# Kernel optimization log

Hardware: AMD Instinct MI355X
Metric: run time of the kernel (lower is better)

Reference implementation:

```python
import jax, jax.numpy as jnp
import numpy as np

MIN_CLUSTERS = 3.0
MAX_CLUSTERS = 50.0


def setup_inputs() -> dict:
    key = jax.random.key(0)
    ks = jax.random.split(key, 12)
    B, N, D = 16, 8192, 256
    E_half = B * N * 16  # avg degree ~32 after symmetrization
    x = jax.random.normal(ks[0], (B, N, D), dtype=jnp.float32)
    mask = jnp.zeros((B, 1, N), dtype=jnp.float32)  # all nodes valid (> -1e8)
    # within-graph random edges, duplicated in both directions (undirected convention)
    g = jax.random.randint(ks[1], (E_half,), 0, B)
    u = jax.random.randint(ks[2], (E_half,), 0, N)
    v = jax.random.randint(ks[3], (E_half,), 0, N)
    src = (g * N + u).astype(jnp.int32)
    dst = (g * N + v).astype(jnp.int32)
    edge_index = jnp.stack([jnp.concatenate([src, dst]), jnp.concatenate([dst, src])])
    batch_vec = jnp.repeat(jnp.arange(B, dtype=jnp.int32), N)
    x_graph = jax.random.normal(ks[4], (B * N, 64), dtype=jnp.float32)
    in_dim = 3 * D + 5  # 773
    W1 = jax.random.normal(ks[5], (in_dim, 64), dtype=jnp.float32) * 0.02
    b1 = jnp.zeros((64,), dtype=jnp.float32)
    W2 = jax.random.normal(ks[6], (64, 32), dtype=jnp.float32) * 0.02
    b2 = jnp.zeros((32,), dtype=jnp.float32)
    W3 = jax.random.normal(ks[7], (32, 1), dtype=jnp.float32) * 0.02
    b3 = jnp.zeros((1,), dtype=jnp.float32)
    return {"x": x, "mask": mask, "x_graph": x_graph, "edge_index": edge_index,
            "batch_vec": batch_vec, "W1": W1, "b1": b1, "W2": W2, "b2": b2,
            "W3": W3, "b3": b3}


def reference(x, mask, x_graph, edge_index, batch_vec, W1, b1, W2, b2, W3, b3):
    B, N, D = x.shape
    valid = mask[:, 0, :] > -1e8  # [B, N] bool
    vf = valid.astype(x.dtype)
    node_counts = vf.sum(axis=1)               # [B]
    safe_nc = jnp.maximum(node_counts, 1.0)
    max_allowed = jnp.minimum(safe_nc, MAX_CLUSTERS)
    min_allowed = jnp.minimum(max_allowed, MIN_CLUSTERS)

    # masked pooled node-feature stats (mean / max / unbiased std)
    cnt = node_counts[:, None]                  # [B,1]
    x_mean = (x * vf[:, :, None]).sum(axis=1) / jnp.maximum(cnt, 1.0)
    x_max = jnp.where(valid[:, :, None], x, -jnp.inf).max(axis=1)
    x_max = jnp.where(cnt > 0, x_max, 0.0)
    diff = (x - x_mean[:, None, :]) * vf[:, :, None]
    var = (diff * diff).sum(axis=1) / jnp.maximum(cnt - 1.0, 1.0)
    x_std = jnp.where(cnt > 1, jnp.sqrt(var), 0.0)

    # structural features: degree histogram via one segment_sum over edge endpoints
    src, dst = edge_index[0], edge_index[1]
    total_nodes = batch_vec.shape[0]
    same = (batch_vec[src] == batch_vec[dst]).astype(x.dtype)
    deg = jax.ops.segment_sum(same, src, num_segments=total_nodes)  # per-node degree
    nodes_per_graph = jax.ops.segment_sum(jnp.ones((total_nodes,), x.dtype), batch_vec, num_segments=B)
    E_b = jax.ops.segment_sum(same, batch_vec[src], num_segments=B)
    num_edges = jnp.floor(E_b / 2.0)  # edge_index duplicated both directions -> E//2
    deg_sum = jax.ops.segment_sum(deg, batch_vec, num_segments=B)
    deg_sq = jax.ops.segment_sum(deg * deg, batch_vec, num_segments=B)
    deg_max = jax.ops.segment_max(deg, batch_vec, num_segments=B)
    npg = jnp.maximum(nodes_per_graph, 1.0)
    deg_mean = deg_sum / npg
    deg_var = (deg_sq - nodes_per_graph * deg_mean * deg_mean) / jnp.maximum(nodes_per_graph - 1.0, 1.0)
    deg_std = jnp.sqrt(jnp.maximum(deg_var, 0.0))

    nc = node_counts
    max_edges = nc * (nc - 1.0) / 2.0
    has = (E_b > 0) & (nc > 1)
    density = jnp.where(has, num_edges / jnp.maximum(max_edges, 1.0), 0.0)
    avg_degree = jnp.where(has, deg_mean / 10.0, 0.0)
    max_degree = jnp.where(has, deg_max / jnp.maximum(nc, 1.0), 0.0)
    degree_std = jnp.where(has & (nodes_per_graph > 1), deg_std / 10.0, 0.0)
    log_size = jnp.log(nc + 1.0) / 5.0
    structural = jnp.stack([log_size, density, avg_degree, max_degree, degree_std], axis=1)

    gf = jnp.concatenate([x_mean, x_max, x_std, structural], axis=1)  # [B, 3D+5]
    h = jax.nn.relu(gf @ W1 + b1)          # dropout is identity at inference
    h = jax.nn.relu(h @ W2 + b2)
    score = jax.nn.sigmoid(h @ W3 + b3)[:, 0]

    ncc = MIN_CLUSTERS + score * (MAX_CLUSTERS - MIN_CLUSTERS)
    ncc = jnp.maximum(jnp.minimum(ncc, max_allowed), min_allowed)
    rounded = jnp.round(ncc)
    max_batch_clusters = max_allowed.min().astype(jnp.int32)
    num_clusters_final = jnp.clip(rounded.mean().astype(jnp.int32), 1, max_batch_clusters)
    cluster_ratio = (ncc / safe_nc).mean()
    return num_clusters_final, cluster_ratio
```

## Files before the change

kernel.cpp:

```cpp
#include <hip/hip_runtime.h>
#include <math.h>

#define BATCH  16
#define NDIM   8192
#define NSHIFT 13
#define DDIM   256
#define NS2    64
#define TCNT   81


__global__ void __launch_bounds__(512) k_edge(
        const int* __restrict__ e0, const int* __restrict__ e1,
        const int* __restrict__ bv, int* __restrict__ gacc,
        unsigned char* __restrict__ hist, int E, int ce, int NH, int total_nodes) {
    __shared__ unsigned hloc[16384];
    __shared__ int sflag;
    int tid = threadIdx.x, bid = blockIdx.x;
    if (bid == 0 && tid < 128) gacc[tid] = 0;
    if (tid == 0) sflag = 0;
    #pragma unroll
    for (int i = 0; i < 32; ++i) hloc[tid + 512 * i] = 0u;
    {
        const int4* bv4 = (const int4*)bv;
        int n4 = total_nodes >> 2;
        int bad = 0;
        for (int i = tid; i < n4; i += 512) {
            int4 v = bv4[i];
            int g = (i * 4) >> NSHIFT;
            bad |= (v.x ^ g) | (v.y ^ g) | (v.z ^ g) | (v.w ^ g);
        }
        if (bad) atomicOr(&sflag, 1);
    }
    __syncthreads();
    bool fp = (sflag == 0);
    int h = bid % NH, c = bid / NH;
    int start = c * ce;
    int end = start + ce; if (end > E) end = E;
    if (fp) {
        for (int e = start + tid * 4; e + 3 < end; e += 512 * 4) {
            int4 s4 = *(const int4*)(e0 + e);
            int4 d4 = *(const int4*)(e1 + e);
            if ((s4.x >> NSHIFT) == (d4.x >> NSHIFT) && (s4.x >> 16) == h)
                atomicAdd(&hloc[(s4.x & 65535) >> 2], 1u << ((s4.x & 3) * 8));
            if ((s4.y >> NSHIFT) == (d4.y >> NSHIFT) && (s4.y >> 16) == h)
                atomicAdd(&hloc[(s4.y & 65535) >> 2], 1u << ((s4.y & 3) * 8));
            if ((s4.z >> NSHIFT) == (d4.z >> NSHIFT) && (s4.z >> 16) == h)
                atomicAdd(&hloc[(s4.z & 65535) >> 2], 1u << ((s4.z & 3) * 8));
            if ((s4.w >> NSHIFT) == (d4.w >> NSHIFT) && (s4.w >> 16) == h)
                atomicAdd(&hloc[(s4.w & 65535) >> 2], 1u << ((s4.w & 3) * 8));
        }
    } else {
        for (int e = start + tid * 4; e + 3 < end; e += 512 * 4) {
            int4 s4 = *(const int4*)(e0 + e);
            int4 d4 = *(const int4*)(e1 + e);
            if (bv[s4.x] == bv[d4.x] && (s4.x >> 16) == h)
                atomicAdd(&hloc[(s4.x & 65535) >> 2], 1u << ((s4.x & 3) * 8));
            if (bv[s4.y] == bv[d4.y] && (s4.y >> 16) == h)
                atomicAdd(&hloc[(s4.y & 65535) >> 2], 1u << ((s4.y & 3) * 8));
            if (bv[s4.z] == bv[d4.z] && (s4.z >> 16) == h)
                atomicAdd(&hloc[(s4.z & 65535) >> 2], 1u << ((s4.z & 3) * 8));
            if (bv[s4.w] == bv[d4.w] && (s4.w >> 16) == h)
                atomicAdd(&hloc[(s4.w & 65535) >> 2], 1u << ((s4.w & 3) * 8));
        }
    }
    __syncthreads();
    uint4* dst = (uint4*)(hist + (size_t)c * ((size_t)NH * 65536) + (size_t)h * 65536);
    const uint4* src = (const uint4*)hloc;
    #pragma unroll
    for (int i = 0; i < 8; ++i) dst[tid + 512 * i] = src[tid + 512 * i];
}

__global__ void __launch_bounds__(256) k_work(
        const unsigned char* __restrict__ hist, const int* __restrict__ bv,
        const float* __restrict__ x, const float* __restrict__ mask,
        float* __restrict__ part, int* __restrict__ vcarr, int* __restrict__ gacc,
        int total_nodes, int NCHUNK, int NH, int MRGB) {
    __shared__ float4 Ls[256], Lq[256], Lm[256];
    __shared__ unsigned pk[4][64][8];
    __shared__ int ls[BATCH], lq[BATCH], lm[BATCH], lc[BATCH], lvc;
    int t = threadIdx.x;
    if ((int)blockIdx.x < MRGB) {
        if (t < BATCH) { ls[t] = 0; lq[t] = 0; lm[t] = 0; lc[t] = 0; }
        int cg = t >> 6, col = t & 63;
        int gcol = blockIdx.x * 64 + col;
        int nCol = total_nodes >> 4;
        unsigned a0=0,a1=0,a2=0,a3=0,b0=0,b1=0,b2=0,b3=0;
        if (gcol < nCol) {
            const uint4* H4 = (const uint4*)hist;
            size_t SB4 = ((size_t)NH * 65536) >> 4;
            #pragma unroll 2
            for (int c = cg; c < NCHUNK; c += 4) {
                uint4 v = H4[(size_t)c * SB4 + gcol];
                a0 += v.x & 0x00FF00FFu; b0 += (v.x >> 8) & 0x00FF00FFu;
                a1 += v.y & 0x00FF00FFu; b1 += (v.y >> 8) & 0x00FF00FFu;
                a2 += v.z & 0x00FF00FFu; b2 += (v.z >> 8) & 0x00FF00FFu;
                a3 += v.w & 0x00FF00FFu; b3 += (v.w >> 8) & 0x00FF00FFu;
            }
        }
        pk[cg][col][0] = a0; pk[cg][col][1] = a1; pk[cg][col][2] = a2; pk[cg][col][3] = a3;
        pk[cg][col][4] = b0; pk[cg][col][5] = b1; pk[cg][col][6] = b2; pk[cg][col][7] = b3;
        __syncthreads();
        int col2 = t >> 2, w = t & 3;
        int node0 = blockIdx.x * 1024 + col2 * 16 + w * 4;
        if (node0 + 3 < total_nodes) {
            unsigned A = pk[0][col2][w]     + pk[1][col2][w]     + pk[2][col2][w]     + pk[3][col2][w];
            unsigned B = pk[0][col2][4 + w] + pk[1][col2][4 + w] + pk[2][col2][4 + w] + pk[3][col2][4 + w];
            int c0 = (int)(A & 0xFFFFu), c2 = (int)(A >> 16);
            int c1 = (int)(B & 0xFFFFu), c3 = (int)(B >> 16);
            int4 bq = ((const int4*)bv)[node0 >> 2];
            if (bq.x == bq.y && bq.x == bq.z && bq.x == bq.w) {
                int b = bq.x;
                int mx = max(max(c0, c1), max(c2, c3));
                atomicAdd(&ls[b], c0 + c1 + c2 + c3);
                atomicAdd(&lq[b], c0 * c0 + c1 * c1 + c2 * c2 + c3 * c3);
                atomicMax(&lm[b], mx);
                atomicAdd(&lc[b], 4);
            } else {
                int cc[4] = { c0, c1, c2, c3 };
                int bb[4] = { bq.x, bq.y, bq.z, bq.w };
                for (int k = 0; k < 4; ++k) {
                    atomicAdd(&ls[bb[k]], cc[k]);
                    atomicAdd(&lq[bb[k]], cc[k] * cc[k]);
                    atomicMax(&lm[bb[k]], cc[k]);
                    atomicAdd(&lc[bb[k]], 1);
                }
            }
        }
        __syncthreads();
        if (t < BATCH) {
            if (ls[t]) atomicAdd(&gacc[t], ls[t]);
            if (lq[t]) atomicAdd(&gacc[BATCH + t], lq[t]);
            if (lm[t]) atomicMax(&gacc[2 * BATCH + t], lm[t]);
            if (lc[t]) atomicAdd(&gacc[3 * BATCH + t], lc[t]);
        }
    } else {
        int idx = blockIdx.x - MRGB;
        int ns = idx & (NS2 - 1), b = idx / NS2;
        int dbase = (t & 63) * 4, rg = t >> 6;
        int n0 = ns * (NDIM / NS2);
        const float* prow = x + (size_t)b * NDIM * DDIM + (size_t)(n0 + rg) * DDIM + dbase;
        const float* pm   = mask + (size_t)b * NDIM + n0 + rg;
        float s0=0.f,s1=0.f,s2=0.f,s3=0.f;
        float q0=0.f,q1=0.f,q2=0.f,q3=0.f;
        float m0=-INFINITY,m1=-INFINITY,m2=-INFINITY,m3=-INFINITY;
        int vcnt = 0;
        #pragma unroll 2
        for (int k = 0; k < 8; ++k) {
            float4 v0 = *(const float4*)(prow);
            float4 v1 = *(const float4*)(prow + 4 * DDIM);
            float4 v2 = *(const float4*)(prow + 8 * DDIM);
            float4 v3 = *(const float4*)(prow + 12 * DDIM);
            float f0 = (pm[0]  > -1.0e8f) ? 1.f : 0.f;
            float f1 = (pm[4]  > -1.0e8f) ? 1.f : 0.f;
            float f2 = (pm[8]  > -1.0e8f) ? 1.f : 0.f;
            float f3 = (pm[12] > -1.0e8f) ? 1.f : 0.f;
            s0 += v0.x*f0 + v1.x*f1 + v2.x*f2 + v3.x*f3;
            s1 += v0.y*f0 + v1.y*f1 + v2.y*f2 + v3.y*f3;
            s2 += v0.z*f0 + v1.z*f1 + v2.z*f2 + v3.z*f3;
            s3 += v0.w*f0 + v1.w*f1 + v2.w*f2 + v3.w*f3;
            q0 += v0.x*v0.x*f0 + v1.x*v1.x*f1 + v2.x*v2.x*f2 + v3.x*v3.x*f3;
            q1 += v0.y*v0.y*f0 + v1.y*v1.y*f1 + v2.y*v2.y*f2 + v3.y*v3.y*f3;
            q2 += v0.z*v0.z*f0 + v1.z*v1.z*f1 + v2.z*v2.z*f2 + v3.z*v3.z*f3;
            q3 += v0.w*v0.w*f0 + v1.w*v1.w*f1 + v2.w*v2.w*f2 + v3.w*v3.w*f3;
            if (f0 > 0.f) { m0=fmaxf(m0,v0.x); m1=fmaxf(m1,v0.y); m2=fmaxf(m2,v0.z); m3=fmaxf(m3,v0.w); }
            if (f1 > 0.f) { m0=fmaxf(m0,v1.x); m1=fmaxf(m1,v1.y); m2=fmaxf(m2,v1.z); m3=fmaxf(m3,v1.w); }
            if (f2 > 0.f) { m0=fmaxf(m0,v2.x); m1=fmaxf(m1,v2.y); m2=fmaxf(m2,v2.z); m3=fmaxf(m3,v2.w); }
            if (f3 > 0.f) { m0=fmaxf(m0,v3.x); m1=fmaxf(m1,v3.y); m2=fmaxf(m2,v3.z); m3=fmaxf(m3,v3.w); }
            vcnt += (int)f0 + (int)f1 + (int)f2 + (int)f3;
            prow += 16 * DDIM;
            pm   += 16;
        }
        if (t == 0) lvc = 0;
        Ls[t] = make_float4(s0, s1, s2, s3);
        Lq[t] = make_float4(q0, q1, q2, q3);
        Lm[t] = make_float4(m0, m1, m2, m3);
        __syncthreads();
        if ((t & 63) == 0 && vcnt) atomicAdd(&lvc, vcnt);
        if (t < 64) {
            float4 S = Ls[t], Q = Lq[t], M = Lm[t];
            #pragma unroll
            for (int r = 1; r < 4; ++r) {
                float4 a = Ls[t + 64 * r];
                S.x += a.x; S.y += a.y; S.z += a.z; S.w += a.w;
                a = Lq[t + 64 * r];
                Q.x += a.x; Q.y += a.y; Q.z += a.z; Q.w += a.w;
                a = Lm[t + 64 * r];
                M.x = fmaxf(M.x, a.x); M.y = fmaxf(M.y, a.y);
                M.z = fmaxf(M.z, a.z); M.w = fmaxf(M.w, a.w);
            }
            size_t base = ((size_t)(b * NS2 + ns) * 3) * DDIM;
            *(float4*)(part + base + 0 * DDIM + 4 * t) = S;
            *(float4*)(part + base + 1 * DDIM + 4 * t) = Q;
            *(float4*)(part + base + 2 * DDIM + 4 * t) = M;
        }
        __syncthreads();
        if (t == 0) vcarr[idx] = lvc;
    }
}

__global__ void __launch_bounds__(256) k_tail(
        const float* __restrict__ part, const int* __restrict__ vcarr,
        int* __restrict__ gacc,
        const float* __restrict__ W1, const float* __restrict__ B1,
        const float* __restrict__ W2, const float* __restrict__ B2,
        const float* __restrict__ W3, const float* __restrict__ B3,
        float* __restrict__ sc, float* __restrict__ out) {
    __shared__ float  sg[768];
    __shared__ float  sst[5];
    __shared__ float4 sacc[256];
    __shared__ float  sh1[64];
    __shared__ float  sh2[32];
    __shared__ int    svc[64];
    int b = blockIdx.x, t = threadIdx.x;

    if (t < 64) svc[t] = vcarr[b * 64 + t];
    float s = 0.f, q = 0.f, m = -INFINITY;
    #pragma unroll 4
    for (int ns = 0; ns < NS2; ++ns) {
        size_t base = ((size_t)(b * NS2 + ns) * 3) * DDIM;
        s += part[base + t];
        q += part[base + DDIM + t];
        m = fmaxf(m, part[base + 2 * DDIM + t]);
    }
    __syncthreads();
    if (t == 0) {
        int c = 0;
        #pragma unroll
        for (int i = 0; i < 64; ++i) c += svc[i];
        svc[0] = c;
    }
    __syncthreads();
    float cnt  = (float)svc[0];
    float mean = s / fmaxf(cnt, 1.f);
    float xmax = (cnt > 0.f) ? m : 0.f;
    float var  = (q - 2.f * mean * s + mean * mean * cnt) / fmaxf(cnt - 1.f, 1.f);
    float xstd = (cnt > 1.f) ? sqrtf(fmaxf(var, 0.f)) : 0.f;
    sg[t]       = mean;
    sg[256 + t] = xmax;
    sg[512 + t] = xstd;
    if (t == 0) {
        float nc   = cnt;
        float npg  = (float)gacc[3 * BATCH + b];
        float Eb   = (float)gacc[b];
        float dsq  = (float)gacc[BATCH + b];
        float dmx  = (float)gacc[2 * BATCH + b];
        float num_edges = floorf(Eb * 0.5f);
        float npg_s = fmaxf(npg, 1.f);
        float dmean = Eb / npg_s;
        float dvar  = (dsq - npg * dmean * dmean) / fmaxf(npg - 1.f, 1.f);
        float dstd  = sqrtf(fmaxf(dvar, 0.f));
        bool  has   = (Eb > 0.f) && (nc > 1.f);
        float mxe   = nc * (nc - 1.f) * 0.5f;
        sst[0] = logf(nc + 1.f) * 0.2f;
        sst[1] = has ? num_edges / fmaxf(mxe, 1.f) : 0.f;
        sst[2] = has ? dmean * 0.1f : 0.f;
        sst[3] = has ? dmx / fmaxf(nc, 1.f) : 0.f;
        sst[4] = (has && npg > 1.f) ? dstd * 0.1f : 0.f;
    }
    __syncthreads();

    int jq = t & 15, k = t >> 4;
    const float4* W = (const float4*)W1;
    float4 a = make_float4(0.f, 0.f, 0.f, 0.f);
    for (int i = k; i < 768; i += 16) {
        float4 w = W[i * 16 + jq];
        float gv = sg[i];
        a.x += gv * w.x; a.y += gv * w.y; a.z += gv * w.z; a.w += gv * w.w;
    }
    if (k == 0) {
        #pragma unroll
        for (int mm = 0; mm < 5; ++mm) {
            float4 w = W[(768 + mm) * 16 + jq];
            float gv = sst[mm];
            a.x += gv * w.x; a.y += gv * w.y; a.z += gv * w.z; a.w += gv * w.w;
        }
    }
    sacc[t] = a;
    __syncthreads();
    for (int stp = 128; stp >= 16; stp >>= 1) {
        if (t < stp) {
            float4 o = sacc[t + stp];
            sacc[t].x += o.x; sacc[t].y += o.y; sacc[t].z += o.z; sacc[t].w += o.w;
        }
        __syncthreads();
    }
    if (t < 16) {
        float4 r = sacc[t];
        float4 bb = ((const float4*)B1)[t];
        sh1[4*t+0] = fmaxf(r.x + bb.x, 0.f);
        sh1[4*t+1] = fmaxf(r.y + bb.y, 0.f);
        sh1[4*t+2] = fmaxf(r.z + bb.z, 0.f);
        sh1[4*t+3] = fmaxf(r.w + bb.w, 0.f);
    }
    __syncthreads();

    if (t < 32) {
        float acc = B2[t];
        #pragma unroll 8
        for (int i = 0; i < 64; ++i) acc += sh1[i] * W2[i * 32 + t];
        sh2[t] = fmaxf(acc, 0.f);
    }
    __syncthreads();

    if (t == 0) {
        float acc = B3[0];
        #pragma unroll 8
        for (int i = 0; i < 32; ++i) acc += sh2[i] * W3[i];
        float score = 1.f / (1.f + expf(-acc));
        float ncc = 3.f + score * 47.f;
        float nc = cnt;
        float safe_nc = fmaxf(nc, 1.f);
        float maxall = fminf(safe_nc, 50.f);
        float minall = fminf(maxall, 3.f);
        ncc = fmaxf(fminf(ncc, maxall), minall);
        __hip_atomic_store(&sc[3*b+0], rintf(ncc),    __ATOMIC_RELEASE, __HIP_MEMORY_SCOPE_AGENT);
        __hip_atomic_store(&sc[3*b+1], ncc / safe_nc, __ATOMIC_RELEASE, __HIP_MEMORY_SCOPE_AGENT);
        __hip_atomic_store(&sc[3*b+2], maxall,        __ATOMIC_RELEASE, __HIP_MEMORY_SCOPE_AGENT);
        int prev = __hip_atomic_fetch_add(&gacc[TCNT], 1, __ATOMIC_ACQ_REL, __HIP_MEMORY_SCOPE_AGENT);
        if (prev == BATCH - 1) {
            float sr = 0.f, sq = 0.f, mm = 1e30f;
            for (int g = 0; g < BATCH; ++g) {
                sr += __hip_atomic_load(&sc[3*g+0], __ATOMIC_ACQUIRE, __HIP_MEMORY_SCOPE_AGENT);
                sq += __hip_atomic_load(&sc[3*g+1], __ATOMIC_ACQUIRE, __HIP_MEMORY_SCOPE_AGENT);
                mm = fminf(mm, __hip_atomic_load(&sc[3*g+2], __ATOMIC_ACQUIRE, __HIP_MEMORY_SCOPE_AGENT));
            }
            int mbc = (int)mm;
            int ncf = (int)(sr / (float)BATCH);
            if (ncf < 1) ncf = 1;
            if (ncf > mbc) ncf = mbc;
            out[0] = (float)ncf;
            out[1] = sq / (float)BATCH;
        }
    }
}

extern "C" void kernel_launch(void* const* d_in, const int* in_sizes, int n_in,
                              void* d_out, int out_size, void* d_ws, size_t ws_size,
                              hipStream_t stream) {
    const float* x    = (const float*)d_in[0];
    const float* mask = (const float*)d_in[1];
    const int*   eidx = (const int*)d_in[3];
    const int*   bv   = (const int*)d_in[4];
    const float* W1   = (const float*)d_in[5];
    const float* B1   = (const float*)d_in[6];
    const float* W2   = (const float*)d_in[7];
    const float* B2   = (const float*)d_in[8];
    const float* W3   = (const float*)d_in[9];
    const float* B3   = (const float*)d_in[10];

    const int total_nodes = in_sizes[4];
    const int E = in_sizes[3] / 2;
    const int NH = (total_nodes + 65535) >> 16;
    const size_t SB = (size_t)NH * 65536;
    const int XS1B = NS2 * BATCH;
    const int MRGB = (total_nodes + 1023) / 1024;

    const size_t PARTB = (size_t)BATCH * NS2 * 3 * DDIM * 4;
    char*  w     = (char*)d_ws;
    int*   gacc  = (int*)w;
    float* sc    = (float*)(w + 1024);
    int*   vcarr = (int*)(w + 2048);
    float* part  = (float*)(w + 65536);
    unsigned char* hist = (unsigned char*)(w + 65536 + PARTB);

    size_t avail = (ws_size > 65536 + PARTB) ? ws_size - 65536 - PARTB : SB;
    int NCHUNK = (int)(avail / SB);
    if (NCHUNK > 128) NCHUNK = 128;
    if (NCHUNK < 1)   NCHUNK = 1;
    int ce = (((E + NCHUNK - 1) / NCHUNK) + 3) & ~3;

    k_edge<<<NCHUNK * NH, 512, 0, stream>>>(eidx, eidx + E, bv, gacc, hist, E, ce, NH,
                                            total_nodes);
    k_work<<<MRGB + XS1B, 256, 0, stream>>>(hist, bv, x, mask, part, vcarr, gacc,
                                            total_nodes, NCHUNK, NH, MRGB);
    k_tail<<<BATCH,       256, 0, stream>>>(part, vcarr, gacc, W1, B1, W2, B2, W3, B3,
                                            sc, (float*)d_out);
}
```

Baseline: 89.29 us.

## Fuse tail MLP into work kernel via last-block counters and atomic-free degree partials

Drops the third kernel launch by having the last x-stats block of each graph run the MLP tail, after spinning on a counter until all degree-merge blocks have finished. The degree-histogram merge now writes per-window partial stats, using a block tree reduction when the window covers one graph, in place of shared and global atomics. The tail then reduces these partials. It also handles leftover edges in k1. This saves launch overhead and a global atomic round but adds spin-wait risk and serialized tail work per graph.

```diff
diff --git a/kernel.cpp b/kernel.cpp
--- a/kernel.cpp
+++ b/kernel.cpp
@@ -6,20 +6,18 @@
 #define NSHIFT 13
 #define DDIM   256
 #define NS2    64
-#define TCNT   81
-
-
-__global__ void __launch_bounds__(512) k_edge(
+
+
+__global__ void __launch_bounds__(512) k1(
         const int* __restrict__ e0, const int* __restrict__ e1,
-        const int* __restrict__ bv, int* __restrict__ gacc,
-        unsigned char* __restrict__ hist, int E, int ce, int NH, int total_nodes) {
+        const int* __restrict__ bv, unsigned char* __restrict__ hist,
+        unsigned* __restrict__ ctr, int E, int ce, int NH, int total_nodes) {
     __shared__ unsigned hloc[16384];
-    __shared__ int sflag;
-    int tid = threadIdx.x, bid = blockIdx.x;
-    if (bid == 0 && tid < 128) gacc[tid] = 0;
-    if (tid == 0) sflag = 0;
-    #pragma unroll
-    for (int i = 0; i < 32; ++i) hloc[tid + 512 * i] = 0u;
+    int tid = threadIdx.x, wg = blockIdx.x;
+    if (wg == 0 && tid < 32) ctr[tid] = 0u;
+
+    if (tid == 0) hloc[0] = 0u;
+    __syncthreads();
     {
         const int4* bv4 = (const int4*)bv;
         int n4 = total_nodes >> 2;
@@ -29,11 +27,17 @@
             int g = (i * 4) >> NSHIFT;
             bad |= (v.x ^ g) | (v.y ^ g) | (v.z ^ g) | (v.w ^ g);
         }
-        if (bad) atomicOr(&sflag, 1);
-    }
-    __syncthreads();
-    bool fp = (sflag == 0);
-    int h = bid % NH, c = bid / NH;
+        if (bad) atomicOr(&hloc[0], 1u);
+    }
+    __syncthreads();
+    bool fp = (hloc[0] == 0u);
+    __syncthreads();
+
+    #pragma unroll
+    for (int i = 0; i < 32; ++i) hloc[tid + 512 * i] = 0u;
+    __syncthreads();
+
+    int h = wg % NH, c = wg / NH;
     int start = c * ce;
     int end = start + ce; if (end > E) end = E;
     if (fp) {
@@ -63,79 +67,107 @@
                 atomicAdd(&hloc[(s4.w & 65535) >> 2], 1u << ((s4.w & 3) * 8));
         }
     }
-    __syncthreads();
+    if (tid == 0) {
+        for (int e = end & ~3; e < end; ++e) {
+            int s = e0[e], d = e1[e];
+            bool same = fp ? ((s >> NSHIFT) == (d >> NSHIFT)) : (bv[s] == bv[d]);
+            if (same && (s >> 16) == h)
+                atomicAdd(&hloc[(s & 65535) >> 2], 1u << ((s & 3) * 8));
+        }
+    }
+    __syncthreads();
+
     uint4* dst = (uint4*)(hist + (size_t)c * ((size_t)NH * 65536) + (size_t)h * 65536);
     const uint4* src = (const uint4*)hloc;
     #pragma unroll
     for (int i = 0; i < 8; ++i) dst[tid + 512 * i] = src[tid + 512 * i];
 }
 
-__global__ void __launch_bounds__(256) k_work(
+__global__ void __launch_bounds__(256) k2(
+        const float* __restrict__ x, const float* __restrict__ mask,
         const unsigned char* __restrict__ hist, const int* __restrict__ bv,
-        const float* __restrict__ x, const float* __restrict__ mask,
-        float* __restrict__ part, int* __restrict__ vcarr, int* __restrict__ gacc,
-        int total_nodes, int NCHUNK, int NH, int MRGB) {
+        int* __restrict__ mpart, float* __restrict__ part,
+        int* __restrict__ vcarr, unsigned* __restrict__ ctr,
+        const float* __restrict__ W1, const float* __restrict__ B1,
+        const float* __restrict__ W2, const float* __restrict__ B2,
+        const float* __restrict__ W3, const float* __restrict__ B3,
+        float* __restrict__ sc, float* __restrict__ out,
+        int total_nodes, int NCH, int NH, int MRGB, int nwin) {
     __shared__ float4 Ls[256], Lq[256], Lm[256];
-    __shared__ unsigned pk[4][64][8];
-    __shared__ int ls[BATCH], lq[BATCH], lm[BATCH], lc[BATCH], lvc;
+    __shared__ int lvc;
+    __shared__ unsigned sprev;
     int t = threadIdx.x;
-    if ((int)blockIdx.x < MRGB) {
-        if (t < BATCH) { ls[t] = 0; lq[t] = 0; lm[t] = 0; lc[t] = 0; }
-        int cg = t >> 6, col = t & 63;
-        int gcol = blockIdx.x * 64 + col;
-        int nCol = total_nodes >> 4;
-        unsigned a0=0,a1=0,a2=0,a3=0,b0=0,b1=0,b2=0,b3=0;
-        if (gcol < nCol) {
-            const uint4* H4 = (const uint4*)hist;
-            size_t SB4 = ((size_t)NH * 65536) >> 4;
-            #pragma unroll 2
-            for (int c = cg; c < NCHUNK; c += 4) {
-                uint4 v = H4[(size_t)c * SB4 + gcol];
-                a0 += v.x & 0x00FF00FFu; b0 += (v.x >> 8) & 0x00FF00FFu;
-                a1 += v.y & 0x00FF00FFu; b1 += (v.y >> 8) & 0x00FF00FFu;
-                a2 += v.z & 0x00FF00FFu; b2 += (v.z >> 8) & 0x00FF00FFu;
-                a3 += v.w & 0x00FF00FFu; b3 += (v.w >> 8) & 0x00FF00FFu;
+    int bid = blockIdx.x;
+
+    if (bid < MRGB) {
+        int* r = (int*)Ls;
+        int* redS = r, * redQ = r + 256, * redM = r + 512;
+        int* mstat = r + 768;
+        unsigned* uflag = (unsigned*)(r + 840);
+        int w = bid;
+        if (t == 0) *uflag = 0u;
+        if (t < 64) mstat[t] = 0;
+        __syncthreads();
+        int ui = w * 256 + t;
+        size_t strideU = (size_t)NH * 16384;
+        const unsigned* base = (const unsigned*)hist + (size_t)(ui >> 14) * 16384 + (ui & 16383);
+        unsigned lo = 0, hi = 0;
+        #pragma unroll 4
+        for (int c = 0; c < NCH; ++c) {
+            unsigned v = base[(size_t)c * strideU];
+            lo += v & 0x00FF00FFu; hi += (v >> 8) & 0x00FF00FFu;
+        }
+        int c0 = (int)(lo & 0xFFFFu), c2 = (int)(lo >> 16);
+        int c1 = (int)(hi & 0xFFFFu), c3 = (int)(hi >> 16);
+        int4 bq = ((const int4*)bv)[ui];
+        int g0 = bv[w << 10];
+        if (!(bq.x == g0 && bq.y == g0 && bq.z == g0 && bq.w == g0))
+            atomicOr(uflag, 1u);
+        __syncthreads();
+        if (*uflag == 0u) {
+            redS[t] = c0 + c1 + c2 + c3;
+            redQ[t] = c0*c0 + c1*c1 + c2*c2 + c3*c3;
+            redM[t] = max(max(c0, c1), max(c2, c3));
+            __syncthreads();
+            for (int st = 128; st > 0; st >>= 1) {
+                if (t < st) {
+                    redS[t] += redS[t + st];
+                    redQ[t] += redQ[t + st];
+                    redM[t]  = max(redM[t], redM[t + st]);
+                }
+                __syncthreads();
             }
-        }
-        pk[cg][col][0] = a0; pk[cg][col][1] = a1; pk[cg][col][2] = a2; pk[cg][col][3] = a3;
-        pk[cg][col][4] = b0; pk[cg][col][5] = b1; pk[cg][col][6] = b2; pk[cg][col][7] = b3;
-        __syncthreads();
-        int col2 = t >> 2, w = t & 3;
-        int node0 = blockIdx.x * 1024 + col2 * 16 + w * 4;
-        if (node0 + 3 < total_nodes) {
-            unsigned A = pk[0][col2][w]     + pk[1][col2][w]     + pk[2][col2][w]     + pk[3][col2][w];
-            unsigned B = pk[0][col2][4 + w] + pk[1][col2][4 + w] + pk[2][col2][4 + w] + pk[3][col2][4 + w];
-            int c0 = (int)(A & 0xFFFFu), c2 = (int)(A >> 16);
-            int c1 = (int)(B & 0xFFFFu), c3 = (int)(B >> 16);
-            int4 bq = ((const int4*)bv)[node0 >> 2];
-            if (bq.x == bq.y && bq.x == bq.z && bq.x == bq.w) {
-                int b = bq.x;
-                int mx = max(max(c0, c1), max(c2, c3));
-                atomicAdd(&ls[b], c0 + c1 + c2 + c3);
-                atomicAdd(&lq[b], c0 * c0 + c1 * c1 + c2 * c2 + c3 * c3);
-                atomicMax(&lm[b], mx);
-                atomicAdd(&lc[b], 4);
-            } else {
-                int cc[4] = { c0, c1, c2, c3 };
-                int bb[4] = { bq.x, bq.y, bq.z, bq.w };
-                for (int k = 0; k < 4; ++k) {
-                    atomicAdd(&ls[bb[k]], cc[k]);
-                    atomicAdd(&lq[bb[k]], cc[k] * cc[k]);
-                    atomicMax(&lm[bb[k]], cc[k]);
-                    atomicAdd(&lc[bb[k]], 1);
+            if (t < 64) {
+                int g = t >> 2, k = t & 3;
+                int v = 0;
+                if (g == g0) v = (k == 0) ? redS[0] : (k == 1) ? redQ[0]
+                              : (k == 2) ? redM[0] : 1024;
+                mpart[w * 64 + t] = v;
+            }
+        } else {
+            int cc4[4] = { c0, c1, c2, c3 };
+            int bb4[4] = { bq.x, bq.y, bq.z, bq.w };
+            for (int k = 0; k < 4; ++k) {
+                if ((unsigned)bb4[k] < 16u) {
+                    atomicAdd(&mstat[bb4[k] * 4 + 0], cc4[k]);
+                    atomicAdd(&mstat[bb4[k] * 4 + 1], cc4[k] * cc4[k]);
+                    atomicMax(&mstat[bb4[k] * 4 + 2], cc4[k]);
+                    atomicAdd(&mstat[bb4[k] * 4 + 3], 1);
                 }
             }
-        }
-        __syncthreads();
-        if (t < BATCH) {
-            if (ls[t]) atomicAdd(&gacc[t], ls[t]);
-            if (lq[t]) atomicAdd(&gacc[BATCH + t], lq[t]);
-            if (lm[t]) atomicMax(&gacc[2 * BATCH + t], lm[t]);
-            if (lc[t]) atomicAdd(&gacc[3 * BATCH + t], lc[t]);
-        }
-    } else {
-        int idx = blockIdx.x - MRGB;
-        int ns = idx & (NS2 - 1), b = idx / NS2;
+            __syncthreads();
+            if (t < 64) mpart[w * 64 + t] = mstat[t];
+        }
+        if (t == 0) {
+            __threadfence();
+            __hip_atomic_fetch_add(&ctr[16], 1u, __ATOMIC_ACQ_REL, __HIP_MEMORY_SCOPE_AGENT);
+        }
+        return;
+    }
+
+    int idx = bid - MRGB;
+    int ns = idx & (NS2 - 1), b = idx / NS2;
+    {
         int dbase = (t & 63) * 4, rg = t >> 6;
         int n0 = ns * (NDIM / NS2);
         const float* prow = x + (size_t)b * NDIM * DDIM + (size_t)(n0 + rg) * DDIM + dbase;
@@ -196,33 +228,61 @@
         __syncthreads();
         if (t == 0) vcarr[idx] = lvc;
     }
-}
-
-__global__ void __launch_bounds__(256) k_tail(
-        const float* __restrict__ part, const int* __restrict__ vcarr,
-        int* __restrict__ gacc,
-        const float* __restrict__ W1, const float* __restrict__ B1,
-        const float* __restrict__ W2, const float* __restrict__ B2,
-        const float* __restrict__ W3, const float* __restrict__ B3,
-        float* __restrict__ sc, float* __restrict__ out) {
-    __shared__ float  sg[768];
-    __shared__ float  sst[5];
-    __shared__ float4 sacc[256];
-    __shared__ float  sh1[64];
-    __shared__ float  sh2[32];
-    __shared__ int    svc[64];
-    int b = blockIdx.x, t = threadIdx.x;
+
+    __syncthreads();
+    if (t == 0) {
+        __threadfence();
+        sprev = __hip_atomic_fetch_add(&ctr[b], 1u, __ATOMIC_ACQ_REL,
+                                       __HIP_MEMORY_SCOPE_AGENT);
+    }
+    __syncthreads();
+    if (sprev != 63u) return;
+    if (t == 0) {
+        while (__hip_atomic_load(&ctr[16], __ATOMIC_ACQUIRE,
+                                 __HIP_MEMORY_SCOPE_AGENT) < (unsigned)MRGB)
+            __builtin_amdgcn_s_sleep(8);
+        __threadfence();
+    }
+    __syncthreads();
+
+    float*  sg   = (float*)Ls;
+    float4* sacc = Lq;
+    float*  b3l  = (float*)Lm;
+    float*  sh1  = b3l;
+    float*  sh2  = b3l + 64;
+    float*  sst  = b3l + 96;
+    int*    svc  = (int*)(b3l + 104);
+    int*    dS   = (int*)(b3l + 168);
+    int*    dQ   = dS + 128;
+    int*    dM   = dQ + 128;
+    int*    dC   = dM + 128;
 
     if (t < 64) svc[t] = vcarr[b * 64 + t];
+    int eS = 0, eQ = 0, eM = 0, eC = 0;
+    if (t < 128) {
+        for (int w = t; w < nwin; w += 128) {
+            int4 v = ((const int4*)mpart)[w * 16 + b];
+            eS += v.x; eQ += v.y; eM = max(eM, v.z); eC += v.w;
+        }
+    }
     float s = 0.f, q = 0.f, m = -INFINITY;
     #pragma unroll 4
-    for (int ns = 0; ns < NS2; ++ns) {
-        size_t base = ((size_t)(b * NS2 + ns) * 3) * DDIM;
+    for (int nn = 0; nn < NS2; ++nn) {
+        size_t base = ((size_t)(b * NS2 + nn) * 3) * DDIM;
         s += part[base + t];
         q += part[base + DDIM + t];
         m = fmaxf(m, part[base + 2 * DDIM + t]);
     }
     __syncthreads();
+    if (t < 128) { dS[t] = eS; dQ[t] = eQ; dM[t] = eM; dC[t] = eC; }
+    __syncthreads();
+    for (int st = 64; st > 0; st >>= 1) {
+        if (t < st) {
+            dS[t] += dS[t + st]; dQ[t] += dQ[t + st];
+            dM[t] = max(dM[t], dM[t + st]); dC[t] += dC[t + st];
+        }
+        __syncthreads();
+    }
     if (t == 0) {
         int c = 0;
         #pragma unroll
@@ -240,10 +300,10 @@
     sg[512 + t] = xstd;
     if (t == 0) {
         float nc   = cnt;
-        float npg  = (float)gacc[3 * BATCH + b];
-        float Eb   = (float)gacc[b];
-        float dsq  = (float)gacc[BATCH + b];
-        float dmx  = (float)gacc[2 * BATCH + b];
+        float npg  = (float)dC[0];
+        float Eb   = (float)dS[0];
+        float dsq  = (float)dQ[0];
+        float dmx  = (float)dM[0];
         float num_edges = floorf(Eb * 0.5f);
         float npg_s = fmaxf(npg, 1.f);
         float dmean = Eb / npg_s;
@@ -259,15 +319,15 @@
     }
     __syncthreads();
 
-    int jq = t & 15, k = t >> 4;
+    int jq = t & 15, kk = t >> 4;
     const float4* W = (const float4*)W1;
     float4 a = make_float4(0.f, 0.f, 0.f, 0.f);
-    for (int i = k; i < 768; i += 16) {
+    for (int i = kk; i < 768; i += 16) {
         float4 w = W[i * 16 + jq];
         float gv = sg[i];
         a.x += gv * w.x; a.y += gv * w.y; a.z += gv * w.z; a.w += gv * w.w;
     }
-    if (k == 0) {
+    if (kk == 0) {
         #pragma unroll
         for (int mm = 0; mm < 5; ++mm) {
             float4 w = W[(768 + mm) * 16 + jq];
@@ -316,8 +376,9 @@
         __hip_atomic_store(&sc[3*b+0], rintf(ncc),    __ATOMIC_RELEASE, __HIP_MEMORY_SCOPE_AGENT);
         __hip_atomic_store(&sc[3*b+1], ncc / safe_nc, __ATOMIC_RELEASE, __HIP_MEMORY_SCOPE_AGENT);
         __hip_atomic_store(&sc[3*b+2], maxall,        __ATOMIC_RELEASE, __HIP_MEMORY_SCOPE_AGENT);
-        int prev = __hip_atomic_fetch_add(&gacc[TCNT], 1, __ATOMIC_ACQ_REL, __HIP_MEMORY_SCOPE_AGENT);
-        if (prev == BATCH - 1) {
+        unsigned prev = __hip_atomic_fetch_add(&ctr[17], 1u, __ATOMIC_ACQ_REL,
+                                               __HIP_MEMORY_SCOPE_AGENT);
+        if (prev == (unsigned)(BATCH - 1)) {
             float sr = 0.f, sq = 0.f, mm = 1e30f;
             for (int g = 0; g < BATCH; ++g) {
                 sr += __hip_atomic_load(&sc[3*g+0], __ATOMIC_ACQUIRE, __HIP_MEMORY_SCOPE_AGENT);
@@ -352,27 +413,28 @@
     const int E = in_sizes[3] / 2;
     const int NH = (total_nodes + 65535) >> 16;
     const size_t SB = (size_t)NH * 65536;
-    const int XS1B = NS2 * BATCH;
-    const int MRGB = (total_nodes + 1023) / 1024;
+    const int nwin = total_nodes >> 10;
+    const int MRGB = nwin;
 
     const size_t PARTB = (size_t)BATCH * NS2 * 3 * DDIM * 4;
     char*  w     = (char*)d_ws;
-    int*   gacc  = (int*)w;
-    float* sc    = (float*)(w + 1024);
-    int*   vcarr = (int*)(w + 2048);
+    unsigned* ctr = (unsigned*)w;
+    float* sc    = (float*)(w + 4096);
+    int*   mpart = (int*)(w + 8192);
+    int*   vcarr = (int*)(w + 49152);
     float* part  = (float*)(w + 65536);
     unsigned char* hist = (unsigned char*)(w + 65536 + PARTB);
 
     size_t avail = (ws_size > 65536 + PARTB) ? ws_size - 65536 - PARTB : SB;
-    int NCHUNK = (int)(avail / SB);
-    if (NCHUNK > 128) NCHUNK = 128;
-    if (NCHUNK < 1)   NCHUNK = 1;
-    int ce = (((E + NCHUNK - 1) / NCHUNK) + 3) & ~3;
-
-    k_edge<<<NCHUNK * NH, 512, 0, stream>>>(eidx, eidx + E, bv, gacc, hist, E, ce, NH,
-                                            total_nodes);
-    k_work<<<MRGB + XS1B, 256, 0, stream>>>(hist, bv, x, mask, part, vcarr, gacc,
-                                            total_nodes, NCHUNK, NH, MRGB);
-    k_tail<<<BATCH,       256, 0, stream>>>(part, vcarr, gacc, W1, B1, W2, B2, W3, B3,
-                                            sc, (float*)d_out);
+    int NCH = (int)(avail / SB);
+    if (NCH > 128) NCH = 128;
+    if (NCH < 1)   NCH = 1;
+    int ce = (((E + NCH - 1) / NCH) + 3) & ~3;
+
+    k1<<<NCH * NH,           512, 0, stream>>>(eidx, eidx + E, bv, hist, ctr,
+                                               E, ce, NH, total_nodes);
+    k2<<<MRGB + NS2 * BATCH, 256, 0, stream>>>(x, mask, hist, bv, mpart, part,
+                                               vcarr, ctr, W1, B1, W2, B2, W3, B3,
+                                               sc, (float*)d_out,
+                                               total_nodes, NCH, NH, MRGB, nwin);
 }
```

New measurement: 152.1 us. 1.7x slower.
